# Performance work log

Hardware: AMD Instinct MI355X
Metric: run time of the kernel (lower is better)

## Reference

```python
import jax, jax.numpy as jnp
import numpy as np

N = 64
D_MODEL = 512
L_MAX = 2048
BATCH = 8
DT_MIN, DT_MAX = 1e-3, 1e-1


def _make_s4_buffers(n):
    r = np.arange(1, n + 1, dtype=np.float64)
    # hippo[i,j] = sqrt(2(i+1)+1)*sqrt(2(j+1)+1) if i>j, (i+1)+1 on diag, else 0
    hippo = np.where(r[:, None] > r[None, :],
                     np.sqrt(2 * r[:, None] + 1.0) * np.sqrt(2 * r[None, :] + 1.0),
                     0.0)
    hippo = hippo + np.diag(r + 1.0)
    nhippo = -hippo
    p = 0.5 * np.sqrt(2.0 * r + 1.0)
    q = 2.0 * p
    S = nhippo + p[:, None] * q[None, :]
    lmbda, V = np.linalg.eig(S)
    Vc = V.conj().T
    p = Vc @ p
    q = Vc @ q.conj()
    return (p.astype(np.complex64), q.astype(np.complex64), lmbda.astype(np.complex64))


def setup_inputs() -> dict:
    key = jax.random.key(0)
    ku, kb, kc, ks = jax.random.split(key, 4)
    u = jax.random.normal(ku, (BATCH, L_MAX, D_MODEL), dtype=jnp.float32)
    std = float(np.sqrt(2.0 / (N + D_MODEL)))  # xavier_normal for (n, d_model)
    B = jax.random.normal(kb, (D_MODEL, N), dtype=jnp.float32) * std
    Ct = jax.random.normal(kc, (D_MODEL, N), dtype=jnp.float32) * std
    D = jnp.ones((D_MODEL,), dtype=jnp.float32)
    scale = float(np.log(DT_MAX) - np.log(DT_MIN))
    log_step = jax.random.uniform(ks, (D_MODEL,), dtype=jnp.float32) * scale + float(np.log(DT_MIN))
    p, q, lmbda = _make_s4_buffers(N)
    omega_l = np.exp(2j * np.pi / L_MAX * np.arange(L_MAX)).astype(np.complex64)
    return {"u": u, "B": B, "Ct": Ct, "D": D, "log_step": log_step,
            "p": jnp.asarray(p), "q": jnp.asarray(q), "lmbda": jnp.asarray(lmbda),
            "omega_l": jnp.asarray(omega_l)}


def _s4_kernel(B, Ct, log_step, p, q, lmbda, omega_l):
    L = omega_l.shape[0]
    step = jnp.exp(log_step)                                   # [d]
    g = jnp.outer(2.0 / step, (1.0 - omega_l) / (1.0 + omega_l))  # [d, L] complex
    c = 2.0 / (1.0 + omega_l)                                  # [L]
    # shared Cauchy resolvent: 1/(g - lambda), [d, L, n]
    r = 1.0 / (g[:, :, None] - lmbda)
    a0 = jnp.conj(Ct)  # [d, n]
    a1 = jnp.conj(q)   # [n]
    k00 = jnp.einsum('dn,dln->dl', a0 * B, r)
    k01 = jnp.einsum('dn,dln->dl', a0 * p, r)
    k10 = jnp.einsum('dn,dln->dl', a1 * B, r)
    k11 = jnp.einsum('n,dln->dl', a1 * p, r)
    at_roots = c * (k00 - k01 * (1.0 / (1.0 + k11)) * k10)     # [d, L]
    Kf = jnp.fft.ifft(at_roots, n=L, axis=-1)
    order = (-jnp.arange(L)) % L                               # [0, L-1, ..., 1]
    return Kf[:, order].real                                   # [d, L] float32


def reference(u, B, Ct, D, log_step, p, q, lmbda, omega_l):
    L = u.shape[1]
    K = _s4_kernel(B, Ct, log_step, p, q, lmbda, omega_l)      # [d, L]
    # non-circular FFT convolution
    ud = jnp.fft.rfft(jnp.pad(u, ((0, 0), (0, L), (0, 0))), axis=1)   # [B, L+1, d]
    Kd = jnp.fft.rfft(jnp.pad(K, ((0, 0), (0, L))), axis=-1)          # [d, L+1]
    y = jnp.fft.irfft(ud.transpose(0, 2, 1) * Kd, axis=-1)[..., :L]   # [B, d, L]
    return y.transpose(0, 2, 1) + D[None, None, :] * u
```

## Files before the change

### kernel.cpp

```cpp
#include <hip/hip_runtime.h>
#include <hip/hip_bf16.h>

#define NT 256
#define R2f 0.70710678118654752f
#define CS1 0.92387953251128674f
#define SN1 0.38268343236508978f
#define PI2 6.2831853071795865f

__device__ __forceinline__ float2 cmulf(float2 a, float2 b) {
    return make_float2(a.x * b.x - a.y * b.y, a.x * b.y + a.y * b.x);
}
__device__ __forceinline__ float2 cadd(float2 a, float2 b) { return make_float2(a.x + b.x, a.y + b.y); }
__device__ __forceinline__ float2 csub(float2 a, float2 b) { return make_float2(a.x - b.x, a.y - b.y); }

template<bool INV>
__device__ __forceinline__ float2 tww(float2 v, float wx, float wy) {
    float sy = INV ? -wy : wy;
    return make_float2(v.x * wx - v.y * sy, v.x * sy + v.y * wx);
}
template<bool INV>
__device__ __forceinline__ float2 mul_mi(float2 v) {
    return INV ? make_float2(-v.y, v.x) : make_float2(v.y, -v.x);
}

template<bool INV>
__device__ __forceinline__ void dft4(float2& a, float2& b, float2& c, float2& d) {
    float2 t0 = cadd(a, c), t1 = csub(a, c);
    float2 t2 = cadd(b, d), t3 = csub(b, d);
    float2 jt3 = mul_mi<INV>(t3);
    a = cadd(t0, t2);
    c = csub(t0, t2);
    b = cadd(t1, jt3);
    d = csub(t1, jt3);
}

template<bool INV>
__device__ __forceinline__ void fft16(float2 v[16]) {
    dft4<INV>(v[0], v[4], v[8],  v[12]);
    dft4<INV>(v[1], v[5], v[9],  v[13]);
    dft4<INV>(v[2], v[6], v[10], v[14]);
    dft4<INV>(v[3], v[7], v[11], v[15]);
    v[5]  = tww<INV>(v[5],  CS1, -SN1);
    v[9]  = tww<INV>(v[9],  R2f, -R2f);
    v[13] = tww<INV>(v[13], SN1, -CS1);
    v[6]  = tww<INV>(v[6],  R2f, -R2f);
    v[10] = mul_mi<INV>(v[10]);
    v[14] = tww<INV>(v[14], -R2f, -R2f);
    v[7]  = tww<INV>(v[7],  SN1, -CS1);
    v[11] = tww<INV>(v[11], -R2f, -R2f);
    v[15] = tww<INV>(v[15], -CS1,  SN1);
    dft4<INV>(v[0],  v[1],  v[2],  v[3]);
    dft4<INV>(v[4],  v[5],  v[6],  v[7]);
    dft4<INV>(v[8],  v[9],  v[10], v[11]);
    dft4<INV>(v[12], v[13], v[14], v[15]);
    float2 t;
    t = v[1];  v[1]  = v[4];  v[4]  = t;
    t = v[2];  v[2]  = v[8];  v[8]  = t;
    t = v[3];  v[3]  = v[12]; v[12] = t;
    t = v[6];  v[6]  = v[9];  v[9]  = t;
    t = v[7];  v[7]  = v[13]; v[13] = t;
    t = v[11]; v[11] = v[14]; v[14] = t;
}

template<bool INV>
__device__ __forceinline__ void twchain(float2 v[16], float ang) {
    float s, c;
    __sincosf(INV ? ang : -ang, &s, &c);
    float2 w = make_float2(c, s);
    float2 t = w;
    v[1] = cmulf(v[1], t);
    #pragma unroll
    for (int a = 2; a < 16; ++a) { t = cmulf(t, w); v[a] = cmulf(v[a], t); }
}

template<bool INV>
__device__ void fft4096(float2 v[16], float2* lds, int tid) {
    const int hi = tid >> 4, lo = tid & 15;
    if (!INV) {
        fft16<false>(v);
        twchain<false>(v, PI2 * (float)tid * (1.0f / 4096.0f));
        __syncthreads();
        #pragma unroll
        for (int a = 0; a < 16; ++a) lds[tid + 256 * a] = v[a];
        __syncthreads();
        #pragma unroll
        for (int m1 = 0; m1 < 16; ++m1) v[m1] = lds[(m1 * 16 + lo) + 256 * hi];
        fft16<false>(v);
        twchain<false>(v, PI2 * (float)lo * (1.0f / 256.0f));
        __syncthreads();
        #pragma unroll
        for (int b = 0; b < 16; ++b) { int e = lo + 16 * b + 256 * hi; lds[e ^ b] = v[b]; }
        __syncthreads();
        #pragma unroll
        for (int m0 = 0; m0 < 16; ++m0) { int e = m0 + 16 * lo + 256 * hi; v[m0] = lds[e ^ lo]; }
        fft16<false>(v);
    } else {
        fft16<true>(v);
        __syncthreads();
        #pragma unroll
        for (int m0 = 0; m0 < 16; ++m0) { int e = m0 + 16 * lo + 256 * hi; lds[e ^ lo] = v[m0]; }
        __syncthreads();
        #pragma unroll
        for (int b = 0; b < 16; ++b) { int e = lo + 16 * b + 256 * hi; v[b] = lds[e ^ b]; }
        twchain<true>(v, PI2 * (float)lo * (1.0f / 256.0f));
        fft16<true>(v);
        __syncthreads();
        #pragma unroll
        for (int m1 = 0; m1 < 16; ++m1) lds[(m1 * 16 + lo) + 256 * hi] = v[m1];
        __syncthreads();
        #pragma unroll
        for (int a = 0; a < 16; ++a) v[a] = lds[tid + 256 * a];
        twchain<true>(v, PI2 * (float)tid * (1.0f / 4096.0f));
        fft16<true>(v);
    }
}

__global__ __launch_bounds__(256) void cauchy_kernel(
    const float* __restrict__ Bmat, const float* __restrict__ Ct,
    const float* __restrict__ log_step,
    const float2* __restrict__ p, const float2* __restrict__ q,
    const float2* __restrict__ lmbda, const float2* __restrict__ omega,
    float2* __restrict__ at)
{
    __shared__ float4 wA[64];
    __shared__ float4 wB[64];
    const int tid = threadIdx.x;
    const int d = blockIdx.x >> 2;
    const int lbase = (blockIdx.x & 3) << 9;

    if (tid < 64) {
        float b  = Bmat[d * 64 + tid];
        float ct = Ct[d * 64 + tid];
        float2 pp = p[tid], qq = q[tid];
        float2 lam = lmbda[tid];
        wA[tid] = make_float4(lam.x, lam.y, ct * b, qq.x * pp.x + qq.y * pp.y);
        wB[tid] = make_float4(ct * pp.x, ct * pp.y, b * qq.x, b * qq.y);
    }
    __syncthreads();

    const float two_over_dt = 2.0f * __expf(-log_step[d]);

    float gx[2], gy[2], ccx[2], ccy[2];
    float S00x[2], S00y[2], Sax[2], Say[2], Sbx[2], Sby[2];
    float Scx[2], Scy[2], Sdx[2], Sdy[2], S11x[2], S11y[2];

    #pragma unroll
    for (int il = 0; il < 2; ++il) {
        int l = lbase + tid + 256 * il;
        float2 om = omega[l];
        float dnx = 1.0f + om.x, dny = om.y;
        float id2 = __builtin_amdgcn_rcpf(dnx * dnx + dny * dny);
        float ivx = dnx * id2, ivy = -dny * id2;
        ccx[il] = 2.0f * ivx; ccy[il] = 2.0f * ivy;
        float nmx = 1.0f - om.x, nmy = -om.y;
        gx[il] = two_over_dt * (nmx * ivx - nmy * ivy);
        gy[il] = two_over_dt * (nmx * ivy + nmy * ivx);
        S00x[il] = 0.f; S00y[il] = 0.f; Sax[il] = 0.f; Say[il] = 0.f;
        Sbx[il] = 0.f; Sby[il] = 0.f; Scx[il] = 0.f; Scy[il] = 0.f;
        Sdx[il] = 0.f; Sdy[il] = 0.f; S11x[il] = 0.f; S11y[il] = 0.f;
    }

    #pragma unroll 4
    for (int n = 0; n < 64; ++n) {
        float4 A  = wA[n];
        float4 Bw = wB[n];
        #pragma unroll
        for (int il = 0; il < 2; ++il) {
            float dx  = gx[il] - A.x;
            float dy  = gy[il] - A.y;
            float ir  = __builtin_amdgcn_rcpf(fmaf(dx, dx, dy * dy));
            float rx  = dx * ir;
            float ry  = -dy * ir;
            S00x[il] = fmaf(A.z,  rx, S00x[il]); S00y[il] = fmaf(A.z,  ry, S00y[il]);
            S11x[il] = fmaf(A.w,  rx, S11x[il]); S11y[il] = fmaf(A.w,  ry, S11y[il]);
            Sax[il]  = fmaf(Bw.x, rx, Sax[il]);  Say[il]  = fmaf(Bw.x, ry, Say[il]);
            Sbx[il]  = fmaf(Bw.y, rx, Sbx[il]);  Sby[il]  = fmaf(Bw.y, ry, Sby[il]);
            Scx[il]  = fmaf(Bw.z, rx, Scx[il]);  Scy[il]  = fmaf(Bw.z, ry, Scy[il]);
            Sdx[il]  = fmaf(Bw.w, rx, Sdx[il]);  Sdy[il]  = fmaf(Bw.w, ry, Sdy[il]);
        }
    }

    #pragma unroll
    for (int il = 0; il < 2; ++il) {
        float k01x = Sax[il] - Sby[il], k01y = Say[il] + Sbx[il];
        float k10x = Scx[il] + Sdy[il], k10y = Scy[il] - Sdx[il];
        float ntx = k01x * k10x - k01y * k10y;
        float nty = k01x * k10y + k01y * k10x;
        float ox = 1.0f + S11x[il], oy = S11y[il];
        float oid = __builtin_amdgcn_rcpf(ox * ox + oy * oy);
        float tx = (ntx * ox + nty * oy) * oid;
        float ty = (nty * ox - ntx * oy) * oid;
        float inx = S00x[il] - tx, iny = S00y[il] - ty;
        int l = lbase + tid + 256 * il;
        at[((size_t)d << 11) | l] =
            make_float2(ccx[il] * inx - ccy[il] * iny, ccx[il] * iny + ccy[il] * inx);
    }
}

__global__ __launch_bounds__(256) void khat_kernel(
    const float2* __restrict__ at, float2* __restrict__ Khat)
{
    __shared__ float2 lds[4096];
    const int tid = threadIdx.x;
    const int d = blockIdx.x;
    const int hi = tid >> 4, lo = tid & 15;
    float2 v[16];

    const float2* ap = at + ((size_t)d << 11);
    #pragma unroll
    for (int n2 = 0; n2 < 8; ++n2) v[n2] = ap[tid + 256 * n2];
    #pragma unroll
    for (int n2 = 8; n2 < 16; ++n2) v[n2] = make_float2(0.f, 0.f);

    fft4096<false>(v, lds, tid);

    float* ldsf = (float*)lds;
    __syncthreads();
    if (!(hi & 1)) {
        int a2 = hi >> 1;
        #pragma unroll
        for (int c = 0; c < 16; ++c) {
            int j = 128 * c + 8 * lo + a2;
            ldsf[j ^ ((j >> 5) & 3)] = v[c].x * (1.0f / (2048.0f * 4096.0f));
        }
    }
    __syncthreads();
    #pragma unroll
    for (int n2 = 0; n2 < 8; ++n2) {
        int j = tid + 256 * n2;
        v[n2] = make_float2(ldsf[j ^ ((j >> 5) & 3)], 0.f);
    }
    #pragma unroll
    for (int n2 = 8; n2 < 16; ++n2) v[n2] = make_float2(0.f, 0.f);

    fft4096<false>(v, lds, tid);

    float2* op = Khat + ((size_t)d << 12);
    #pragma unroll
    for (int c = 0; c < 16; ++c) op[c * 256 + tid] = v[c];
}

__global__ __launch_bounds__(256) void transpose_pack_kernel(
    const float* __restrict__ u, float2* __restrict__ z)
{
    __shared__ float2 tile[64][65];
    int blk = blockIdx.x;
    int lt  = blk & 31;
    int dt8 = (blk >> 5) & 7;
    int bp  = blk >> 8;
    const size_t ub0 = (size_t)(2 * bp) * 2048 * 512;
    const size_t ub1 = (size_t)(2 * bp + 1) * 2048 * 512;
    for (int r = 0; r < 16; ++r) {
        int idx = threadIdx.x + 256 * r;
        int row = idx >> 6;
        int col = idx & 63;
        size_t off = (size_t)(lt * 64 + row) * 512 + (dt8 * 64 + col);
        tile[col][row] = make_float2(u[ub0 + off], u[ub1 + off]);
    }
    __syncthreads();
    for (int r = 0; r < 16; ++r) {
        int idx = threadIdx.x + 256 * r;
        int row = idx >> 6;
        int col = idx & 63;
        z[((size_t)(bp * 512 + dt8 * 64 + row)) * 2048 + lt * 64 + col] = tile[row][col];
    }
}

__global__ __launch_bounds__(256) void conv_kernel(
    float2* __restrict__ z, const float2* __restrict__ Khat,
    const float* __restrict__ D)
{
    __shared__ float2 lds[4096];
    const int tid = threadIdx.x;
    const int d  = blockIdx.x & 511;
    const int bp = blockIdx.x >> 9;
    float2 v[16];
    float2 u0[8];

    float2* zr = z + ((size_t)(bp * 512 + d)) * 2048;
    #pragma unroll
    for (int n2 = 0; n2 < 8; ++n2) { u0[n2] = zr[tid + 256 * n2]; v[n2] = u0[n2]; }
    #pragma unroll
    for (int n2 = 8; n2 < 16; ++n2) v[n2] = make_float2(0.f, 0.f);

    fft4096<false>(v, lds, tid);

    const float2* kh = Khat + ((size_t)d << 12);
    #pragma unroll
    for (int c = 0; c < 16; ++c) v[c] = cmulf(v[c], kh[c * 256 + tid]);

    fft4096<true>(v, lds, tid);

    const float Dd = D[d];
    #pragma unroll
    for (int n2 = 0; n2 < 8; ++n2) {
        zr[tid + 256 * n2] =
            make_float2(v[n2].x + Dd * u0[n2].x, v[n2].y + Dd * u0[n2].y);
    }
}

__global__ __launch_bounds__(256) void untranspose_kernel(
    const float2* __restrict__ yz, float* __restrict__ out)
{
    __shared__ float2 tile[64][65];
    int blk = blockIdx.x;
    int lt  = blk & 31;
    int dt8 = (blk >> 5) & 7;
    int bp  = blk >> 8;
    for (int r = 0; r < 16; ++r) {
        int idx = threadIdx.x + 256 * r;
        int row = idx >> 6;
        int col = idx & 63;
        float2 vv = yz[((size_t)(bp * 512 + dt8 * 64 + row)) * 2048 + lt * 64 + col];
        tile[col][row] = vv;
    }
    __syncthreads();
    const size_t ub0 = (size_t)(2 * bp) * 2048 * 512;
    const size_t ub1 = (size_t)(2 * bp + 1) * 2048 * 512;
    for (int r = 0; r < 16; ++r) {
        int idx = threadIdx.x + 256 * r;
        int row = idx >> 6;
        int col = idx & 63;
        size_t off = (size_t)(lt * 64 + row) * 512 + (dt8 * 64 + col);
        float2 vv = tile[row][col];
        out[ub0 + off] = vv.x;
        out[ub1 + off] = vv.y;
    }
}

extern "C" void kernel_launch(void* const* d_in, const int* in_sizes, int n_in,
                              void* d_out, int out_size, void* d_ws, size_t ws_size,
                              hipStream_t stream) {
    (void)in_sizes; (void)n_in; (void)out_size; (void)ws_size;
    const float*  u   = (const float*)d_in[0];
    const float*  Bm  = (const float*)d_in[1];
    const float*  Ct  = (const float*)d_in[2];
    const float*  D   = (const float*)d_in[3];
    const float*  ls  = (const float*)d_in[4];
    const float2* p   = (const float2*)d_in[5];
    const float2* q   = (const float2*)d_in[6];
    const float2* lm  = (const float2*)d_in[7];
    const float2* om  = (const float2*)d_in[8];
    float* out = (float*)d_out;

    float2* Khat = (float2*)d_ws;
    float2* z    = (float2*)((char*)d_ws + (size_t)512 * 4096 * 8);
    float2* at   = z;

    hipLaunchKernelGGL(cauchy_kernel, dim3(2048), dim3(256), 0, stream,
                       Bm, Ct, ls, p, q, lm, om, at);
    hipLaunchKernelGGL(khat_kernel, dim3(512), dim3(256), 0, stream, at, Khat);
    hipLaunchKernelGGL(transpose_pack_kernel, dim3(1024), dim3(256), 0, stream, u, z);
    hipLaunchKernelGGL(conv_kernel, dim3(2048), dim3(256), 0, stream, z, Khat, D);
    hipLaunchKernelGGL(untranspose_kernel, dim3(1024), dim3(256), 0, stream, z, out);
}
```

Measured before the change: 105.7 us.

## Exploit conjugate symmetry in Cauchy kernel and specialise half-zero FFT stage

The Cauchy kernel now computes only the first half of the L frequency points (plus the Nyquist point at index 1024) and writes the complex conjugate into the mirrored index. This relies on the real-valued inputs and roots-of-unity symmetry, and halves the grid and the O(d·L·N) resolvent work. The first radix-16 stage of the forward FFT also gets a specialised version that assumes the upper half of its inputs is zero, which removes redundant butterfly arithmetic. The Nyquist point is handled by a single serial thread, which adds a small tail to one block per channel.

Result: faster. 93.16 us (-11.8%).

```diff
diff --git a/kernel.cpp b/kernel.cpp
--- a/kernel.cpp
+++ b/kernel.cpp
@@ -35,11 +35,7 @@
 }
 
 template<bool INV>
-__device__ __forceinline__ void fft16(float2 v[16]) {
-    dft4<INV>(v[0], v[4], v[8],  v[12]);
-    dft4<INV>(v[1], v[5], v[9],  v[13]);
-    dft4<INV>(v[2], v[6], v[10], v[14]);
-    dft4<INV>(v[3], v[7], v[11], v[15]);
+__device__ __forceinline__ void fft16_tail(float2 v[16]) {
     v[5]  = tww<INV>(v[5],  CS1, -SN1);
     v[9]  = tww<INV>(v[9],  R2f, -R2f);
     v[13] = tww<INV>(v[13], SN1, -CS1);
@@ -63,6 +59,28 @@
 }
 
 template<bool INV>
+__device__ __forceinline__ void fft16(float2 v[16]) {
+    dft4<INV>(v[0], v[4], v[8],  v[12]);
+    dft4<INV>(v[1], v[5], v[9],  v[13]);
+    dft4<INV>(v[2], v[6], v[10], v[14]);
+    dft4<INV>(v[3], v[7], v[11], v[15]);
+    fft16_tail<INV>(v);
+}
+
+__device__ __forceinline__ void fft16_hz(float2 v[16]) {
+    #pragma unroll
+    for (int i = 0; i < 4; ++i) {
+        float2 a = v[i], b = v[i + 4];
+        float2 jb = make_float2(b.y, -b.x);
+        v[i]      = cadd(a, b);
+        v[i + 4]  = cadd(a, jb);
+        v[i + 8]  = csub(a, b);
+        v[i + 12] = csub(a, jb);
+    }
+    fft16_tail<false>(v);
+}
+
+template<bool INV>
 __device__ __forceinline__ void twchain(float2 v[16], float ang) {
     float s, c;
     __sincosf(INV ? ang : -ang, &s, &c);
@@ -77,7 +95,7 @@
 __device__ void fft4096(float2 v[16], float2* lds, int tid) {
     const int hi = tid >> 4, lo = tid & 15;
     if (!INV) {
-        fft16<false>(v);
+        fft16_hz(v);
         twchain<false>(v, PI2 * (float)tid * (1.0f / 4096.0f));
         __syncthreads();
         #pragma unroll
@@ -125,8 +143,8 @@
     __shared__ float4 wA[64];
     __shared__ float4 wB[64];
     const int tid = threadIdx.x;
-    const int d = blockIdx.x >> 2;
-    const int lbase = (blockIdx.x & 3) << 9;
+    const int d = blockIdx.x >> 1;
+    const int lbase = (blockIdx.x & 1) << 9;
 
     if (tid < 64) {
         float b  = Bmat[d * 64 + tid];
@@ -139,6 +157,7 @@
     __syncthreads();
 
     const float two_over_dt = 2.0f * __expf(-log_step[d]);
+    float2* atd = at + ((size_t)d << 11);
 
     float gx[2], gy[2], ccx[2], ccy[2];
     float S00x[2], S00y[2], Sax[2], Say[2], Sbx[2], Sby[2];
@@ -192,8 +211,48 @@
         float ty = (nty * ox - ntx * oy) * oid;
         float inx = S00x[il] - tx, iny = S00y[il] - ty;
         int l = lbase + tid + 256 * il;
-        at[((size_t)d << 11) | l] =
-            make_float2(ccx[il] * inx - ccy[il] * iny, ccx[il] * iny + ccy[il] * inx);
+        float2 val = make_float2(ccx[il] * inx - ccy[il] * iny,
+                                 ccx[il] * iny + ccy[il] * inx);
+        atd[l] = val;
+        if (l != 0) atd[2048 - l] = make_float2(val.x, -val.y);
+    }
+
+    if ((blockIdx.x & 1) && tid == 0) {
+        float2 om = omega[1024];
+        float dnx = 1.0f + om.x, dny = om.y;
+        float id2 = __builtin_amdgcn_rcpf(dnx * dnx + dny * dny);
+        float ivx = dnx * id2, ivy = -dny * id2;
+        float cx = 2.0f * ivx, cy = 2.0f * ivy;
+        float nmx = 1.0f - om.x, nmy = -om.y;
+        float ggx = two_over_dt * (nmx * ivx - nmy * ivy);
+        float ggy = two_over_dt * (nmx * ivy + nmy * ivx);
+        float s00x = 0.f, s00y = 0.f, sax = 0.f, say = 0.f, sbx = 0.f, sby = 0.f;
+        float scx = 0.f, scy = 0.f, sdx = 0.f, sdy = 0.f, s11x = 0.f, s11y = 0.f;
+        for (int n = 0; n < 64; ++n) {
+            float4 A  = wA[n];
+            float4 Bw = wB[n];
+            float dx  = ggx - A.x;
+            float dy  = ggy - A.y;
+            float ir  = __builtin_amdgcn_rcpf(fmaf(dx, dx, dy * dy));
+            float rx  = dx * ir;
+            float ry  = -dy * ir;
+            s00x = fmaf(A.z,  rx, s00x); s00y = fmaf(A.z,  ry, s00y);
+            s11x = fmaf(A.w,  rx, s11x); s11y = fmaf(A.w,  ry, s11y);
+            sax  = fmaf(Bw.x, rx, sax);  say  = fmaf(Bw.x, ry, say);
+            sbx  = fmaf(Bw.y, rx, sbx);  sby  = fmaf(Bw.y, ry, sby);
+            scx  = fmaf(Bw.z, rx, scx);  scy  = fmaf(Bw.z, ry, scy);
+            sdx  = fmaf(Bw.w, rx, sdx);  sdy  = fmaf(Bw.w, ry, sdy);
+        }
+        float k01x = sax - sby, k01y = say + sbx;
+        float k10x = scx + sdy, k10y = scy - sdx;
+        float ntx = k01x * k10x - k01y * k10y;
+        float nty = k01x * k10y + k01y * k10x;
+        float ox = 1.0f + s11x, oy = s11y;
+        float oid = __builtin_amdgcn_rcpf(ox * ox + oy * oy);
+        float tx = (ntx * ox + nty * oy) * oid;
+        float ty = (nty * ox - ntx * oy) * oid;
+        float inx = s00x - tx, iny = s00y - ty;
+        atd[1024] = make_float2(cx * inx - cy * iny, cx * iny + cy * inx);
     }
 }
 
@@ -347,7 +406,7 @@
     float2* z    = (float2*)((char*)d_ws + (size_t)512 * 4096 * 8);
     float2* at   = z;
 
-    hipLaunchKernelGGL(cauchy_kernel, dim3(2048), dim3(256), 0, stream,
+    hipLaunchKernelGGL(cauchy_kernel, dim3(1024), dim3(256), 0, stream,
                        Bm, Ct, ls, p, q, lm, om, at);
     hipLaunchKernelGGL(khat_kernel, dim3(512), dim3(256), 0, stream, at, Khat);
     hipLaunchKernelGGL(transpose_pack_kernel, dim3(1024), dim3(256), 0, stream, u, z);
```
